# Performance work log

Hardware: AMD Instinct MI355X
Metric: run time of the kernel (lower is better)

Reference implementation:

```python
import jax, jax.numpy as jnp
import numpy as np

B, N, C = 4, 2048, 1024
H = 16
HD = C // H
SCALE = HD ** -0.5


def setup_inputs() -> dict:
    key = jax.random.key(0)
    ks = jax.random.split(key, 5)
    s = 0.02
    return {
        "x": jax.random.normal(ks[0], (B, N, C), dtype=jnp.float32),
        "w_qkv": jax.random.normal(ks[1], (C, 3 * C), dtype=jnp.float32) * s,
        "b_qkv": jnp.zeros((3 * C,), dtype=jnp.float32),
        "w_proj": jax.random.normal(ks[2], (C, C), dtype=jnp.float32) * s,
        "b_proj": jnp.zeros((C,), dtype=jnp.float32),
    }


def reference(x, w_qkv, b_qkv, w_proj, b_proj):
    b, n, c = x.shape
    qkv = x @ w_qkv + b_qkv                       # [b, n, 3c]
    qkv = qkv.reshape(b, n, 3, H, HD)
    qkv = jnp.transpose(qkv, (2, 0, 3, 1, 4))     # [3, b, h, n, hd]
    q, k, v = qkv[0], qkv[1], qkv[2]
    attn = jnp.einsum("bhqd,bhkd->bhqk", q, k) * SCALE
    attn = jax.nn.softmax(attn, axis=-1)
    out = jnp.einsum("bhqk,bhkd->bhqd", attn, v)  # [b, h, n, hd]
    out = jnp.transpose(out, (0, 2, 1, 3)).reshape(b, n, c)
    return out @ w_proj + b_proj
```

## Files before the change

### kernel.cpp

```cpp
#include <hip/hip_runtime.h>
#include <cstdint>
#include <cstddef>


typedef __attribute__((ext_vector_type(8))) short short8;
typedef __attribute__((ext_vector_type(4))) float f32x4;
typedef _Float16 half4 __attribute__((ext_vector_type(4)));

#if __has_builtin(__builtin_amdgcn_exp2f)
#define EXP2F(x) __builtin_amdgcn_exp2f(x)
#else
#define EXP2F(x) __expf((x) * 0.69314718056f)
#endif

__device__ __forceinline__ short f2bf(float x) {
  unsigned u = __builtin_bit_cast(unsigned, x);
  u += 0x7fffu + ((u >> 16) & 1u);
  return (short)(u >> 16);
}

__device__ __forceinline__ unsigned pkh(float a, float b) {
  auto h = __builtin_amdgcn_cvt_pkrtz(a, b);
  return __builtin_bit_cast(unsigned, h);
}

__device__ __forceinline__ void async16(const void* g, void* l) {
  __builtin_amdgcn_global_load_lds(
      (const __attribute__((address_space(1))) unsigned*)g,
      (__attribute__((address_space(3))) unsigned*)l, 16, 0, 0);
}


__global__ __launch_bounds__(256) void convert_kernel(const float* __restrict__ in,
                                                      short* __restrict__ out) {
  int i = blockIdx.x * 256 + threadIdx.x;
  const float4* p = (const float4*)in + (size_t)i * 2;
  float4 a = p[0], b = p[1];
  short8 r;
  r[0] = f2bf(a.x); r[1] = f2bf(a.y); r[2] = f2bf(a.z); r[3] = f2bf(a.w);
  r[4] = f2bf(b.x); r[5] = f2bf(b.y); r[6] = f2bf(b.z); r[7] = f2bf(b.w);
  *((short8*)out + i) = r;
}

__global__ __launch_bounds__(256) void wtrans_kernel(const float* __restrict__ in,
                                                     short* __restrict__ out,
                                                     int K, int N) {
  __shared__ float tile[32][33];
  int n0 = blockIdx.x * 32, k0 = blockIdx.y * 32;
  int tx = threadIdx.x, ty = threadIdx.y;
  for (int r = ty; r < 32; r += 8)
    tile[r][tx] = in[(size_t)(k0 + r) * N + n0 + tx];
  __syncthreads();
  for (int r = ty; r < 32; r += 8)
    out[(size_t)(n0 + r) * K + k0 + tx] = f2bf(tile[tx][r]);
}


template <int MODE>
__global__ __launch_bounds__(256) void gemm_kernel(
    const short* __restrict__ A, const short* __restrict__ Bt,
    const float* __restrict__ bias, int Nn,
    short* __restrict__ qb, short* __restrict__ kb, short* __restrict__ vtb,
    float* __restrict__ outp) {
  constexpr int K = 1024;
  __shared__ __align__(16) short As[128 * 32];
  __shared__ __align__(16) short Bs[128 * 32];
  const int tid = threadIdx.x, wave = tid >> 6, lane = tid & 63;
  const int quad = lane >> 4, l16 = lane & 15;
  const int m0 = blockIdx.y * 128, n0 = blockIdx.x * 128;
  const int wrow = (wave >> 1) * 64, wcol = (wave & 1) * 64;

  const int str = lane >> 2;
  const int sgc = ((lane & 3) ^ ((lane >> 3) & 3)) * 8;
  const short* Ag = A + (size_t)(m0 + str) * K + sgc;
  const short* Bg = Bt + (size_t)(n0 + str) * K + sgc;

  const int fsw = (l16 >> 1) & 3;

  f32x4 acc[4][4] = {};

  for (int k0 = 0; k0 < K; k0 += 32) {
#pragma unroll
    for (int i = 0; i < 2; ++i) {
      int c = wave * 2 + i;
      async16(Ag + (size_t)c * 16 * K + k0, (char*)As + c * 1024);
      async16(Bg + (size_t)c * 16 * K + k0, (char*)Bs + c * 1024);
    }
    __syncthreads();
    short8 af[4], bf[4];
#pragma unroll
    for (int t = 0; t < 4; ++t) {
      af[t] = *(const short8*)&As[(wrow + t * 16 + l16) * 32 + ((quad ^ fsw) << 3)];
      bf[t] = *(const short8*)&Bs[(wcol + t * 16 + l16) * 32 + ((quad ^ fsw) << 3)];
    }
#pragma unroll
    for (int mt = 0; mt < 4; ++mt)
#pragma unroll
      for (int nt = 0; nt < 4; ++nt)
        acc[mt][nt] = __builtin_amdgcn_mfma_f32_16x16x32_bf16(af[mt], bf[nt],
                                                              acc[mt][nt], 0, 0, 0);
    __syncthreads();
  }

  if (MODE == 0) {
#pragma unroll
    for (int mt = 0; mt < 4; ++mt) {
      int row0 = m0 + wrow + mt * 16 + quad * 4;
      int b = row0 >> 11, n = row0 & 2047;
#pragma unroll
      for (int nt = 0; nt < 4; ++nt) {
        int col = n0 + wcol + nt * 16 + l16;
        float bv = bias[col];
        float v0 = acc[mt][nt][0] + bv, v1 = acc[mt][nt][1] + bv;
        float v2 = acc[mt][nt][2] + bv, v3 = acc[mt][nt][3] + bv;
        int which = col >> 10;
        int h = (col >> 6) & 15;
        int d = col & 63;
        size_t bh = (size_t)(b * 16 + h);
        if (which == 0) {
          const float qs = 0.18033688f;
          size_t base = (bh * 2048 + n) * 64 + d;
          qb[base]       = f2bf(v0 * qs);
          qb[base + 64]  = f2bf(v1 * qs);
          qb[base + 128] = f2bf(v2 * qs);
          qb[base + 192] = f2bf(v3 * qs);
        } else if (which == 1) {
          size_t base = (bh * 2048 + n) * 64 + d;
          kb[base]       = f2bf(v0);
          kb[base + 64]  = f2bf(v1);
          kb[base + 128] = f2bf(v2);
          kb[base + 192] = f2bf(v3);
        } else {
          uint2 pk;
          pk.x = pkh(v0, v1);
          pk.y = pkh(v2, v3);
          *(uint2*)&vtb[(bh * 64 + d) * 2048 + n] = pk;
        }
      }
    }
  } else {
#pragma unroll
    for (int mt = 0; mt < 4; ++mt) {
      int row0 = m0 + wrow + mt * 16 + quad * 4;
#pragma unroll
      for (int nt = 0; nt < 4; ++nt) {
        int col = n0 + wcol + nt * 16 + l16;
        float bv = bias[col];
        outp[(size_t)row0 * Nn + col]       = acc[mt][nt][0] + bv;
        outp[(size_t)(row0 + 1) * Nn + col] = acc[mt][nt][1] + bv;
        outp[(size_t)(row0 + 2) * Nn + col] = acc[mt][nt][2] + bv;
        outp[(size_t)(row0 + 3) * Nn + col] = acc[mt][nt][3] + bv;
      }
    }
  }
}


__global__ __launch_bounds__(256, 4) void attn_kernel(
    const short* __restrict__ qb, const short* __restrict__ kb,
    const short* __restrict__ vtb, short* __restrict__ ob) {
  __shared__ __align__(16) short Ks[2][64 * 64];
  __shared__ __align__(16) short Vs[2][64 * 64];
  __shared__ __align__(16) float Ls[4][32];
  const int tid = threadIdx.x, wave = tid >> 6, lane = tid & 63;
  const int quad = lane >> 4, l16 = lane & 15;
  const int q0 = blockIdx.x * 128;
  const int bh = blockIdx.y;
  const short* Qg = qb + (size_t)bh * (2048 * 64);
  const short* Kg = kb + (size_t)bh * (2048 * 64);
  const short* Vg = vtb + (size_t)bh * (64 * 2048);

  short8 qf[2][2];
#pragma unroll
  for (int qt = 0; qt < 2; ++qt)
#pragma unroll
    for (int kc = 0; kc < 2; ++kc)
      qf[qt][kc] = *(const short8*)
          &Qg[(size_t)(q0 + wave * 32 + qt * 16 + l16) * 64 + kc * 32 + quad * 8];

  const int str = lane >> 3;
  const int sgc = ((lane & 7) ^ (str & 7)) * 8;
  const int fsw = l16 & 7;
  const int c0 = wave * 2, c1 = wave * 2 + 1;

  async16(Kg + (size_t)(c0 * 8 + str) * 64 + sgc, (char*)Ks[0] + c0 * 1024);
  async16(Kg + (size_t)(c1 * 8 + str) * 64 + sgc, (char*)Ks[0] + c1 * 1024);
  async16(Vg + (size_t)(c0 * 8 + str) * 2048 + sgc, (char*)Vs[0] + c0 * 1024);
  async16(Vg + (size_t)(c1 * 8 + str) * 2048 + sgc, (char*)Vs[0] + c1 * 1024);

  float lsum[2] = {0.f, 0.f};
  f32x4 oacc[2][4] = {};

  for (int t = 0; t < 32; ++t) {
    __syncthreads();

    int kvn = (t + 1) * 64;
    if (kvn < 2048) {
      char* kd = (char*)Ks[(t + 1) & 1];
      char* vd = (char*)Vs[(t + 1) & 1];
      async16(Kg + (size_t)(kvn + c0 * 8 + str) * 64 + sgc, kd + c0 * 1024);
      async16(Kg + (size_t)(kvn + c1 * 8 + str) * 64 + sgc, kd + c1 * 1024);
      async16(Vg + (size_t)(c0 * 8 + str) * 2048 + kvn + sgc, vd + c0 * 1024);
      async16(Vg + (size_t)(c1 * 8 + str) * 2048 + kvn + sgc, vd + c1 * 1024);
    }
    const short* Kst = Ks[t & 1];
    const short* Vst = Vs[t & 1];

    f32x4 sacc[2][4] = {};
#pragma unroll
    for (int kc = 0; kc < 2; ++kc) {
      short8 kf[4];
#pragma unroll
      for (int kvt = 0; kvt < 4; ++kvt)
        kf[kvt] = *(const short8*)
            &Kst[(kvt * 16 + l16) * 64 + (((kc * 4 + quad) ^ fsw) << 3)];
#pragma unroll
      for (int kvt = 0; kvt < 4; ++kvt)
#pragma unroll
        for (int qt = 0; qt < 2; ++qt)
          sacc[qt][kvt] = __builtin_amdgcn_mfma_f32_16x16x32_bf16(
              kf[kvt], qf[qt][kc], sacc[qt][kvt], 0, 0, 0);
    }

#pragma unroll
    for (int kvt = 0; kvt < 4; ++kvt) {
      half4 pfr[2];
#pragma unroll
      for (int qt = 0; qt < 2; ++qt) {
        float p0 = EXP2F(sacc[qt][kvt][0]);
        float p1 = EXP2F(sacc[qt][kvt][1]);
        float p2 = EXP2F(sacc[qt][kvt][2]);
        float p3 = EXP2F(sacc[qt][kvt][3]);
        lsum[qt] += (p0 + p1) + (p2 + p3);
        uint2 w;
        w.x = pkh(p0, p1);
        w.y = pkh(p2, p3);
        pfr[qt] = __builtin_bit_cast(half4, w);
      }
      const int vcol = (((kvt * 2 + (quad >> 1)) ^ fsw) << 3) + (quad & 1) * 4;
#pragma unroll
      for (int nt = 0; nt < 4; ++nt) {
        uint2 vr = *(const uint2*)&Vst[(nt * 16 + l16) * 64 + vcol];
        half4 vfr = __builtin_bit_cast(half4, vr);
#pragma unroll
        for (int qt = 0; qt < 2; ++qt)
          oacc[qt][nt] = __builtin_amdgcn_mfma_f32_16x16x16f16(
              pfr[qt], vfr, oacc[qt][nt], 0, 0, 0);
      }
    }
  }

#pragma unroll
  for (int qt = 0; qt < 2; ++qt) {
    float v = lsum[qt];
    v += __shfl_xor(v, 16, 64);
    v += __shfl_xor(v, 32, 64);
    if (quad == 0) Ls[wave][qt * 16 + l16] = v;
  }
  __asm__ volatile("s_waitcnt lgkmcnt(0)" ::: "memory");
  __builtin_amdgcn_wave_barrier();

  const int b = bh >> 4, h = bh & 15;
#pragma unroll
  for (int qt = 0; qt < 2; ++qt) {
    float4 lr = *(const float4*)&Ls[wave][qt * 16 + quad * 4];
    float inv0 = 1.f / lr.x, inv1 = 1.f / lr.y, inv2 = 1.f / lr.z, inv3 = 1.f / lr.w;
#pragma unroll
    for (int nt = 0; nt < 4; ++nt) {
      int d = nt * 16 + l16;
      int qbase = q0 + wave * 32 + qt * 16 + quad * 4;
      size_t obase = ((size_t)(b * 2048 + qbase)) * 1024 + h * 64 + d;
      ob[obase]        = f2bf(oacc[qt][nt][0] * inv0);
      ob[obase + 1024] = f2bf(oacc[qt][nt][1] * inv1);
      ob[obase + 2048] = f2bf(oacc[qt][nt][2] * inv2);
      ob[obase + 3072] = f2bf(oacc[qt][nt][3] * inv3);
    }
  }
}


extern "C" void kernel_launch(void* const* d_in, const int* in_sizes, int n_in,
                              void* d_out, int out_size, void* d_ws, size_t ws_size,
                              hipStream_t stream) {
  const float* x      = (const float*)d_in[0];
  const float* w_qkv  = (const float*)d_in[1];
  const float* b_qkv  = (const float*)d_in[2];
  const float* w_proj = (const float*)d_in[3];
  const float* b_proj = (const float*)d_in[4];
  float* out = (float*)d_out;

  short* xs     = (short*)d_ws;
  short* wqkvT  = xs + (size_t)8192 * 1024;
  short* wprojT = wqkvT + (size_t)3072 * 1024;
  short* qb     = wprojT + (size_t)1024 * 1024;
  short* kb     = qb + (size_t)64 * 2048 * 64;
  short* vtb    = kb + (size_t)64 * 2048 * 64;
  short* aob    = vtb + (size_t)64 * 2048 * 64;

  convert_kernel<<<dim3(4096), 256, 0, stream>>>(x, xs);
  wtrans_kernel<<<dim3(96, 32), dim3(32, 8), 0, stream>>>(w_qkv, wqkvT, 1024, 3072);
  wtrans_kernel<<<dim3(32, 32), dim3(32, 8), 0, stream>>>(w_proj, wprojT, 1024, 1024);

  gemm_kernel<0><<<dim3(24, 64), 256, 0, stream>>>(xs, wqkvT, b_qkv, 3072,
                                                   qb, kb, vtb, nullptr);
  attn_kernel<<<dim3(16, 64), 256, 0, stream>>>(qb, kb, vtb, aob);
  gemm_kernel<1><<<dim3(8, 64), 256, 0, stream>>>(aob, wprojT, b_proj, 1024,
                                                  nullptr, nullptr, nullptr, out);
}
```

Measured before the change: 293.5 us.

## Rework GEMM into 256x128 tiles with triple-buffered async LDS pipeline

The GEMM kernel now uses 512-thread blocks computing 256x128 output tiles with a K-step of 64, triple-buffered shared memory, and async global-to-LDS prefetch two stages ahead. Each iteration is split into two halves so that loads for the next tiles interleave with MFMA work, and s_setprio raises wave priority around the MFMA blocks. This targets global-load latency and barrier stalls in the old single-buffered loop, which synchronized twice per 32-wide K step. The cost is much more LDS per block (about 144 KB), which limits occupancy, and a grid with half as many blocks.

```diff
diff --git a/kernel.cpp b/kernel.cpp
--- a/kernel.cpp
+++ b/kernel.cpp
@@ -57,62 +57,116 @@
 
 
 template <int MODE>
-__global__ __launch_bounds__(256) void gemm_kernel(
+__global__ __launch_bounds__(512, 2) void gemm_kernel(
     const short* __restrict__ A, const short* __restrict__ Bt,
     const float* __restrict__ bias, int Nn,
     short* __restrict__ qb, short* __restrict__ kb, short* __restrict__ vtb,
     float* __restrict__ outp) {
   constexpr int K = 1024;
-  __shared__ __align__(16) short As[128 * 32];
-  __shared__ __align__(16) short Bs[128 * 32];
+  constexpr int NT = K / 64;
+  __shared__ __align__(16) short As[3][256 * 64];
+  __shared__ __align__(16) short Bs[3][128 * 64];
   const int tid = threadIdx.x, wave = tid >> 6, lane = tid & 63;
   const int quad = lane >> 4, l16 = lane & 15;
-  const int m0 = blockIdx.y * 128, n0 = blockIdx.x * 128;
+  const int m0 = blockIdx.y * 256, n0 = blockIdx.x * 128;
   const int wrow = (wave >> 1) * 64, wcol = (wave & 1) * 64;
 
-  const int str = lane >> 2;
-  const int sgc = ((lane & 3) ^ ((lane >> 3) & 3)) * 8;
-  const short* Ag = A + (size_t)(m0 + str) * K + sgc;
-  const short* Bg = Bt + (size_t)(n0 + str) * K + sgc;
-
-  const int fsw = (l16 >> 1) & 3;
+  const int srow = tid >> 3;
+  const int schunk = ((tid & 7) ^ (srow & 7)) * 8;
+  const short* Ag = A + (size_t)(m0 + srow) * K + schunk;
+  const short* Bg = Bt + (size_t)(n0 + srow) * K + schunk;
+  const int fsw = l16 & 7;
 
   f32x4 acc[4][4] = {};
-
-  for (int k0 = 0; k0 < K; k0 += 32) {
-#pragma unroll
-    for (int i = 0; i < 2; ++i) {
-      int c = wave * 2 + i;
-      async16(Ag + (size_t)c * 16 * K + k0, (char*)As + c * 1024);
-      async16(Bg + (size_t)c * 16 * K + k0, (char*)Bs + c * 1024);
-    }
-    __syncthreads();
-    short8 af[4], bf[4];
-#pragma unroll
-    for (int t = 0; t < 4; ++t) {
-      af[t] = *(const short8*)&As[(wrow + t * 16 + l16) * 32 + ((quad ^ fsw) << 3)];
-      bf[t] = *(const short8*)&Bs[(wcol + t * 16 + l16) * 32 + ((quad ^ fsw) << 3)];
-    }
-#pragma unroll
-    for (int mt = 0; mt < 4; ++mt)
-#pragma unroll
-      for (int nt = 0; nt < 4; ++nt)
-        acc[mt][nt] = __builtin_amdgcn_mfma_f32_16x16x32_bf16(af[mt], bf[nt],
-                                                              acc[mt][nt], 0, 0, 0);
-    __syncthreads();
+  short8 af[4][2], bf[2][2];
+
+  auto stageA = [&](int b, int kt) {
+#pragma unroll
+    for (int i = 0; i < 4; ++i)
+      async16(Ag + (size_t)(i * 64) * K + kt * 64,
+              (char*)As[b] + i * 8192 + tid * 16);
+  };
+  auto stageB = [&](int b, int kt) {
+#pragma unroll
+    for (int i = 0; i < 2; ++i)
+      async16(Bg + (size_t)(i * 64) * K + kt * 64,
+              (char*)Bs[b] + i * 8192 + tid * 16);
+  };
+
+  stageA(0, 0); stageB(0, 0);
+  stageA(1, 1); stageB(1, 1);
+  asm volatile("s_waitcnt vmcnt(6)" ::: "memory");
+  __builtin_amdgcn_s_barrier();
+
+  int cb = 0;
+  for (int t = 0; t < NT; ++t) {
+    int sb = cb + 2; if (sb >= 3) sb -= 3;
+    const short* Ab = As[cb];
+    const short* Bb = Bs[cb];
+
+#pragma unroll
+    for (int mf = 0; mf < 4; ++mf)
+#pragma unroll
+      for (int ks = 0; ks < 2; ++ks)
+        af[mf][ks] = *(const short8*)
+            &Ab[(wrow + mf * 16 + l16) * 64 + (((ks * 4 + quad) ^ fsw) << 3)];
+#pragma unroll
+    for (int j = 0; j < 2; ++j)
+#pragma unroll
+      for (int ks = 0; ks < 2; ++ks)
+        bf[j][ks] = *(const short8*)
+            &Bb[(wcol + j * 16 + l16) * 64 + (((ks * 4 + quad) ^ fsw) << 3)];
+    if (t + 2 < NT) stageA(sb, t + 2);
+    __builtin_amdgcn_s_barrier();
+    __builtin_amdgcn_s_setprio(1);
+#pragma unroll
+    for (int ks = 0; ks < 2; ++ks)
+#pragma unroll
+      for (int mf = 0; mf < 4; ++mf)
+#pragma unroll
+        for (int j = 0; j < 2; ++j)
+          acc[mf][j] = __builtin_amdgcn_mfma_f32_16x16x32_bf16(
+              af[mf][ks], bf[j][ks], acc[mf][j], 0, 0, 0);
+    __builtin_amdgcn_s_setprio(0);
+    __builtin_amdgcn_s_barrier();
+
+#pragma unroll
+    for (int j = 0; j < 2; ++j)
+#pragma unroll
+      for (int ks = 0; ks < 2; ++ks)
+        bf[j][ks] = *(const short8*)
+            &Bb[(wcol + (2 + j) * 16 + l16) * 64 + (((ks * 4 + quad) ^ fsw) << 3)];
+    if (t + 2 < NT) stageB(sb, t + 2);
+    __builtin_amdgcn_s_barrier();
+    __builtin_amdgcn_s_setprio(1);
+#pragma unroll
+    for (int ks = 0; ks < 2; ++ks)
+#pragma unroll
+      for (int mf = 0; mf < 4; ++mf)
+#pragma unroll
+        for (int j = 0; j < 2; ++j)
+          acc[mf][2 + j] = __builtin_amdgcn_mfma_f32_16x16x32_bf16(
+              af[mf][ks], bf[j][ks], acc[mf][2 + j], 0, 0, 0);
+    __builtin_amdgcn_s_setprio(0);
+    if (t < NT - 2)
+      asm volatile("s_waitcnt vmcnt(6)" ::: "memory");
+    else if (t == NT - 2)
+      asm volatile("s_waitcnt vmcnt(0)" ::: "memory");
+    __builtin_amdgcn_s_barrier();
+    cb = cb + 1; if (cb >= 3) cb -= 3;
   }
 
   if (MODE == 0) {
 #pragma unroll
-    for (int mt = 0; mt < 4; ++mt) {
-      int row0 = m0 + wrow + mt * 16 + quad * 4;
+    for (int mf = 0; mf < 4; ++mf) {
+      int row0 = m0 + wrow + mf * 16 + quad * 4;
       int b = row0 >> 11, n = row0 & 2047;
 #pragma unroll
-      for (int nt = 0; nt < 4; ++nt) {
-        int col = n0 + wcol + nt * 16 + l16;
+      for (int nf = 0; nf < 4; ++nf) {
+        int col = n0 + wcol + nf * 16 + l16;
         float bv = bias[col];
-        float v0 = acc[mt][nt][0] + bv, v1 = acc[mt][nt][1] + bv;
-        float v2 = acc[mt][nt][2] + bv, v3 = acc[mt][nt][3] + bv;
+        float v0 = acc[mf][nf][0] + bv, v1 = acc[mf][nf][1] + bv;
+        float v2 = acc[mf][nf][2] + bv, v3 = acc[mf][nf][3] + bv;
         int which = col >> 10;
         int h = (col >> 6) & 15;
         int d = col & 63;
@@ -140,16 +194,16 @@
     }
   } else {
 #pragma unroll
-    for (int mt = 0; mt < 4; ++mt) {
-      int row0 = m0 + wrow + mt * 16 + quad * 4;
-#pragma unroll
-      for (int nt = 0; nt < 4; ++nt) {
-        int col = n0 + wcol + nt * 16 + l16;
+    for (int mf = 0; mf < 4; ++mf) {
+      int row0 = m0 + wrow + mf * 16 + quad * 4;
+#pragma unroll
+      for (int nf = 0; nf < 4; ++nf) {
+        int col = n0 + wcol + nf * 16 + l16;
         float bv = bias[col];
-        outp[(size_t)row0 * Nn + col]       = acc[mt][nt][0] + bv;
-        outp[(size_t)(row0 + 1) * Nn + col] = acc[mt][nt][1] + bv;
-        outp[(size_t)(row0 + 2) * Nn + col] = acc[mt][nt][2] + bv;
-        outp[(size_t)(row0 + 3) * Nn + col] = acc[mt][nt][3] + bv;
+        outp[(size_t)row0 * Nn + col]       = acc[mf][nf][0] + bv;
+        outp[(size_t)(row0 + 1) * Nn + col] = acc[mf][nf][1] + bv;
+        outp[(size_t)(row0 + 2) * Nn + col] = acc[mf][nf][2] + bv;
+        outp[(size_t)(row0 + 3) * Nn + col] = acc[mf][nf][3] + bv;
       }
     }
   }
@@ -301,9 +355,9 @@
   wtrans_kernel<<<dim3(96, 32), dim3(32, 8), 0, stream>>>(w_qkv, wqkvT, 1024, 3072);
   wtrans_kernel<<<dim3(32, 32), dim3(32, 8), 0, stream>>>(w_proj, wprojT, 1024, 1024);
 
-  gemm_kernel<0><<<dim3(24, 64), 256, 0, stream>>>(xs, wqkvT, b_qkv, 3072,
+  gemm_kernel<0><<<dim3(24, 32), 512, 0, stream>>>(xs, wqkvT, b_qkv, 3072,
                                                    qb, kb, vtb, nullptr);
   attn_kernel<<<dim3(16, 64), 256, 0, stream>>>(qb, kb, vtb, aob);
-  gemm_kernel<1><<<dim3(8, 64), 256, 0, stream>>>(aob, wprojT, b_proj, 1024,
+  gemm_kernel<1><<<dim3(8, 32), 512, 0, stream>>>(aob, wprojT, b_proj, 1024,
                                                   nullptr, nullptr, nullptr, out);
 }
```

After: 288.4 us. No clear change (-1.7%).

## Triple-buffer GEMM loads with async LDS prefetch, larger QKV tile, XCD-aware block swizzle

Applied to the files above, without the earlier changes.

Rewrites the GEMM mainloop as a 3-stage ring of LDS buffers: loads for tile t+2 are issued before the MFMAs on tile t, and explicit vmcnt waits plus raw barriers replace the two __syncthreads per iteration. The QKV GEMM moves to 256x128 tiles, and block indices are remapped so neighbouring tiles land on the same XCD for L2 reuse; the attention grid gets a similar remap. The aim is to hide global-load latency, cut barrier overhead and improve cache locality. The costs are more LDS and registers per block and hand-tuned waitcnt counts that must match the number of loads issued.

```diff
diff --git a/kernel.cpp b/kernel.cpp
--- a/kernel.cpp
+++ b/kernel.cpp
@@ -28,6 +28,12 @@
   __builtin_amdgcn_global_load_lds(
       (const __attribute__((address_space(1))) unsigned*)g,
       (__attribute__((address_space(3))) unsigned*)l, 16, 0, 0);
+}
+
+__device__ __forceinline__ void barrier_raw() {
+  __asm__ volatile("" ::: "memory");
+  __builtin_amdgcn_s_barrier();
+  __asm__ volatile("" ::: "memory");
 }
 
 
@@ -56,63 +62,99 @@
 }
 
 
-template <int MODE>
-__global__ __launch_bounds__(256) void gemm_kernel(
+template <int BM, int BN, int MODE>
+__global__ __launch_bounds__(256, 2) void gemm_kernel(
     const short* __restrict__ A, const short* __restrict__ Bt,
     const float* __restrict__ bias, int Nn,
     short* __restrict__ qb, short* __restrict__ kb, short* __restrict__ vtb,
     float* __restrict__ outp) {
   constexpr int K = 1024;
-  __shared__ __align__(16) short As[128 * 32];
-  __shared__ __align__(16) short Bs[128 * 32];
+  constexpr int NT = K / 32;
+  constexpr int MR = BM / 32, NR = BN / 32;
+  constexpr int L = (BM + BN) / 64;
+  __shared__ __align__(16) short Ts[3][(BM + BN) * 32];
   const int tid = threadIdx.x, wave = tid >> 6, lane = tid & 63;
   const int quad = lane >> 4, l16 = lane & 15;
-  const int m0 = blockIdx.y * 128, n0 = blockIdx.x * 128;
-  const int wrow = (wave >> 1) * 64, wcol = (wave & 1) * 64;
-
-  const int str = lane >> 2;
-  const int sgc = ((lane & 3) ^ ((lane >> 3) & 3)) * 8;
-  const short* Ag = A + (size_t)(m0 + str) * K + sgc;
-  const short* Bg = Bt + (size_t)(n0 + str) * K + sgc;
-
-  const int fsw = (l16 >> 1) & 3;
-
-  f32x4 acc[4][4] = {};
-
-  for (int k0 = 0; k0 < K; k0 += 32) {
-#pragma unroll
-    for (int i = 0; i < 2; ++i) {
-      int c = wave * 2 + i;
-      async16(Ag + (size_t)c * 16 * K + k0, (char*)As + c * 1024);
-      async16(Bg + (size_t)c * 16 * K + k0, (char*)Bs + c * 1024);
-    }
-    __syncthreads();
-    short8 af[4], bf[4];
-#pragma unroll
-    for (int t = 0; t < 4; ++t) {
-      af[t] = *(const short8*)&As[(wrow + t * 16 + l16) * 32 + ((quad ^ fsw) << 3)];
-      bf[t] = *(const short8*)&Bs[(wcol + t * 16 + l16) * 32 + ((quad ^ fsw) << 3)];
-    }
-#pragma unroll
-    for (int mt = 0; mt < 4; ++mt)
-#pragma unroll
-      for (int nt = 0; nt < 4; ++nt)
-        acc[mt][nt] = __builtin_amdgcn_mfma_f32_16x16x32_bf16(af[mt], bf[nt],
-                                                              acc[mt][nt], 0, 0, 0);
-    __syncthreads();
+
+  const unsigned bid = blockIdx.x + gridDim.x * blockIdx.y;
+  const unsigned c = bid & 7u, j = bid >> 3;
+  const unsigned MC = gridDim.y >> 3;
+  const unsigned chunk = MC * 8u;
+  const unsigned nc = j / chunk, rem = j - nc * chunk;
+  const unsigned m_idx = c * MC + (rem >> 3);
+  const unsigned n_idx = nc * 8u + (rem & 7u);
+  const int m0 = (int)m_idx * BM, n0 = (int)n_idx * BN;
+
+  const int wrow = (wave >> 1) * (BM / 2), wcol = (wave & 1) * (BN / 2);
+
+  const int srow = tid >> 2;
+  const int sch8 = (((tid & 3) ^ (srow & 3)) * 8);
+  const short* Ag = A + (size_t)(m0 + srow) * K + sch8;
+  const short* Bg = Bt + (size_t)(n0 + srow) * K + sch8;
+  const int fq8 = ((quad ^ (l16 & 3)) * 8);
+
+  f32x4 acc[MR][NR] = {};
+
+  auto stage = [&](int b, int kt) {
+    char* dst = (char*)Ts[b] + tid * 16;
+#pragma unroll
+    for (int i = 0; i < BM / 64; ++i)
+      async16(Ag + (size_t)(i * 64) * K + kt * 32, dst + i * 4096);
+#pragma unroll
+    for (int i = 0; i < BN / 64; ++i)
+      async16(Bg + (size_t)(i * 64) * K + kt * 32, dst + (BM / 64 + i) * 4096);
+  };
+
+  stage(0, 0);
+  stage(1, 1);
+  if constexpr (L == 6) asm volatile("s_waitcnt vmcnt(6)" ::: "memory");
+  else                  asm volatile("s_waitcnt vmcnt(4)" ::: "memory");
+  barrier_raw();
+
+  int cb = 0, sb = 2;
+  for (int t = 0; t < NT; ++t) {
+    if (t + 2 < NT) stage(sb, t + 2);
+
+    const short* Tb = Ts[cb];
+    short8 af[MR], bf[NR];
+#pragma unroll
+    for (int mf = 0; mf < MR; ++mf)
+      af[mf] = *(const short8*)&Tb[(wrow + mf * 16 + l16) * 32 + fq8];
+#pragma unroll
+    for (int nf = 0; nf < NR; ++nf)
+      bf[nf] = *(const short8*)&Tb[(BM + wcol + nf * 16 + l16) * 32 + fq8];
+
+    __builtin_amdgcn_s_setprio(1);
+#pragma unroll
+    for (int mf = 0; mf < MR; ++mf)
+#pragma unroll
+      for (int nf = 0; nf < NR; ++nf)
+        acc[mf][nf] = __builtin_amdgcn_mfma_f32_16x16x32_bf16(
+            af[mf], bf[nf], acc[mf][nf], 0, 0, 0);
+    __builtin_amdgcn_s_setprio(0);
+
+    if (t + 2 < NT) {
+      if constexpr (L == 6) asm volatile("s_waitcnt vmcnt(6)" ::: "memory");
+      else                  asm volatile("s_waitcnt vmcnt(4)" ::: "memory");
+    } else {
+      asm volatile("s_waitcnt vmcnt(0)" ::: "memory");
+    }
+    barrier_raw();
+    cb = cb + 1; if (cb >= 3) cb -= 3;
+    sb = sb + 1; if (sb >= 3) sb -= 3;
   }
 
   if (MODE == 0) {
 #pragma unroll
-    for (int mt = 0; mt < 4; ++mt) {
-      int row0 = m0 + wrow + mt * 16 + quad * 4;
+    for (int mf = 0; mf < MR; ++mf) {
+      int row0 = m0 + wrow + mf * 16 + quad * 4;
       int b = row0 >> 11, n = row0 & 2047;
 #pragma unroll
-      for (int nt = 0; nt < 4; ++nt) {
-        int col = n0 + wcol + nt * 16 + l16;
+      for (int nf = 0; nf < NR; ++nf) {
+        int col = n0 + wcol + nf * 16 + l16;
         float bv = bias[col];
-        float v0 = acc[mt][nt][0] + bv, v1 = acc[mt][nt][1] + bv;
-        float v2 = acc[mt][nt][2] + bv, v3 = acc[mt][nt][3] + bv;
+        float v0 = acc[mf][nf][0] + bv, v1 = acc[mf][nf][1] + bv;
+        float v2 = acc[mf][nf][2] + bv, v3 = acc[mf][nf][3] + bv;
         int which = col >> 10;
         int h = (col >> 6) & 15;
         int d = col & 63;
@@ -140,16 +182,16 @@
     }
   } else {
 #pragma unroll
-    for (int mt = 0; mt < 4; ++mt) {
-      int row0 = m0 + wrow + mt * 16 + quad * 4;
-#pragma unroll
-      for (int nt = 0; nt < 4; ++nt) {
-        int col = n0 + wcol + nt * 16 + l16;
+    for (int mf = 0; mf < MR; ++mf) {
+      int row0 = m0 + wrow + mf * 16 + quad * 4;
+#pragma unroll
+      for (int nf = 0; nf < NR; ++nf) {
+        int col = n0 + wcol + nf * 16 + l16;
         float bv = bias[col];
-        outp[(size_t)row0 * Nn + col]       = acc[mt][nt][0] + bv;
-        outp[(size_t)(row0 + 1) * Nn + col] = acc[mt][nt][1] + bv;
-        outp[(size_t)(row0 + 2) * Nn + col] = acc[mt][nt][2] + bv;
-        outp[(size_t)(row0 + 3) * Nn + col] = acc[mt][nt][3] + bv;
+        outp[(size_t)row0 * Nn + col]       = acc[mf][nf][0] + bv;
+        outp[(size_t)(row0 + 1) * Nn + col] = acc[mf][nf][1] + bv;
+        outp[(size_t)(row0 + 2) * Nn + col] = acc[mf][nf][2] + bv;
+        outp[(size_t)(row0 + 3) * Nn + col] = acc[mf][nf][3] + bv;
       }
     }
   }
@@ -164,8 +206,10 @@
   __shared__ __align__(16) float Ls[4][32];
   const int tid = threadIdx.x, wave = tid >> 6, lane = tid & 63;
   const int quad = lane >> 4, l16 = lane & 15;
-  const int q0 = blockIdx.x * 128;
-  const int bh = blockIdx.y;
+  int nlin = blockIdx.x + blockIdx.y * 16;
+  nlin = (nlin & 7) * 128 + (nlin >> 3);
+  const int q0 = (nlin & 15) * 128;
+  const int bh = nlin >> 4;
   const short* Qg = qb + (size_t)bh * (2048 * 64);
   const short* Kg = kb + (size_t)bh * (2048 * 64);
   const short* Vg = vtb + (size_t)bh * (64 * 2048);
@@ -301,9 +345,9 @@
   wtrans_kernel<<<dim3(96, 32), dim3(32, 8), 0, stream>>>(w_qkv, wqkvT, 1024, 3072);
   wtrans_kernel<<<dim3(32, 32), dim3(32, 8), 0, stream>>>(w_proj, wprojT, 1024, 1024);
 
-  gemm_kernel<0><<<dim3(24, 64), 256, 0, stream>>>(xs, wqkvT, b_qkv, 3072,
-                                                   qb, kb, vtb, nullptr);
+  gemm_kernel<256, 128, 0><<<dim3(24, 32), 256, 0, stream>>>(
+      xs, wqkvT, b_qkv, 3072, qb, kb, vtb, nullptr);
   attn_kernel<<<dim3(16, 64), 256, 0, stream>>>(qb, kb, vtb, aob);
-  gemm_kernel<1><<<dim3(8, 64), 256, 0, stream>>>(aob, wprojT, b_proj, 1024,
-                                                  nullptr, nullptr, nullptr, out);
-}
+  gemm_kernel<128, 128, 1><<<dim3(8, 64), 256, 0, stream>>>(
+      aob, wprojT, b_proj, 1024, nullptr, nullptr, nullptr, out);
+}
```

Measured after the change: 276.7 us. 1.06x faster.
